# Optimization experiments

Hardware: AMD Instinct MI355X
Metric: run time of the kernel (lower is better)

Reference implementation:

```python
import jax, jax.numpy as jnp
import numpy as np

L, H, D, DH, DFF, V, P, T, R = 12, 12, 768, 64, 3072, 30522, 512, 2, 50
RAT_LAYER = 6  # original condition: 5 < idx < 7


def layer_norm(x, g, b, eps=1e-12):
    m = x.mean(-1, keepdims=True)
    v = ((x - m) ** 2).mean(-1, keepdims=True)
    return (x - m) / jnp.sqrt(v + eps) * g + b


def setup_inputs() -> dict:
    key = jax.random.key(0)
    ks = iter(jax.random.split(key, 20))
    def n(shape, s=0.02):
        return jax.random.normal(next(ks), shape, dtype=jnp.float32) * s
    inp = dict(
        input_ids=jax.random.randint(next(ks), (4, 512), 0, V, dtype=jnp.int32),
        relations=jax.random.randint(next(ks), (4, 512, 512), 0, R, dtype=jnp.int32),
        attention_mask=jnp.ones((4, 512), dtype=jnp.int32),
        word_emb=n((V, D)), pos_emb=n((P, D)), type_emb=n((T, D)),
        emb_ln_g=jnp.ones((D,)), emb_ln_b=jnp.zeros((D,)),
        Wq=n((L, D, D)), bq=jnp.zeros((L, D)), Wk=n((L, D, D)), bk=jnp.zeros((L, D)),
        Wv=n((L, D, D)), bv=jnp.zeros((L, D)), Wo=n((L, D, D)), bo=jnp.zeros((L, D)),
        ln1_g=jnp.ones((L, D)), ln1_b=jnp.zeros((L, D)),
        Wi=n((L, D, DFF)), bi=jnp.zeros((L, DFF)),
        Wf=n((L, DFF, D)), bf=jnp.zeros((L, D)),
        ln2_g=jnp.ones((L, D)), ln2_b=jnp.zeros((L, D)),
        key_rel=n((L, R, DH)), val_rel=n((L, R, DH)),
        pool_w=n((D, D)), pool_b=jnp.zeros((D,)),
    )
    return inp


def reference(input_ids, relations, attention_mask, word_emb, pos_emb, type_emb,
              emb_ln_g, emb_ln_b, Wq, bq, Wk, bk, Wv, bv, Wo, bo, ln1_g, ln1_b,
              Wi, bi, Wf, bf, ln2_g, ln2_b, key_rel, val_rel, pool_w, pool_b):
    B, S = input_ids.shape
    # BERT embeddings (token_type_ids = zeros as in module default)
    h = word_emb[input_ids] + pos_emb[jnp.arange(S)][None] + type_emb[0][None, None]
    h = layer_norm(h, emb_ln_g, emb_ln_b)
    ext_mask = (1.0 - attention_mask.astype(jnp.float32))[:, None, None, :] * -10000.0
    inv_sqrt_dh = np.float32(1.0 / np.sqrt(DH))
    for i in range(L):
        q = (h @ Wq[i] + bq[i]).reshape(B, S, H, DH).transpose(0, 2, 1, 3)
        k = (h @ Wk[i] + bk[i]).reshape(B, S, H, DH).transpose(0, 2, 1, 3)
        v = (h @ Wv[i] + bv[i]).reshape(B, S, H, DH).transpose(0, 2, 1, 3)
        scores = jnp.einsum('bhsd,bhtd->bhst', q, k)
        if i == RAT_LAYER:
            kr = key_rel[i][relations]            # [B,S,S,DH] gathered relation keys
            scores = scores + jnp.einsum('bhsd,bstd->bhst', q, kr)
        scores = scores * inv_sqrt_dh + ext_mask
        probs = jax.nn.softmax(scores, axis=-1)   # dropout = identity (eval)
        ctx = jnp.einsum('bhst,bhtd->bhsd', probs, v)
        if i == RAT_LAYER:
            vr = val_rel[i][relations]            # [B,S,S,DH] gathered relation values
            ctx = ctx + jnp.einsum('bhst,bstd->bhsd', probs, vr)
        ctx = ctx.transpose(0, 2, 1, 3).reshape(B, S, D)
        attn_out = layer_norm(ctx @ Wo[i] + bo[i] + h, ln1_g[i], ln1_b[i])
        ff = jax.nn.gelu(attn_out @ Wi[i] + bi[i], approximate=False)
        h = layer_norm(ff @ Wf[i] + bf[i] + attn_out, ln2_g[i], ln2_b[i])
    pooled = jnp.tanh(h[:, 0] @ pool_w + pool_b)
    return h, pooled
```

## Files before the change

kernel.cpp:

```cpp
#include <hip/hip_runtime.h>
#include <math.h>

typedef unsigned short u16;
typedef unsigned int   u32;
typedef __bf16  bf16x8 __attribute__((ext_vector_type(8)));
typedef float   f32x4  __attribute__((ext_vector_type(4)));
typedef u16     u16x8  __attribute__((ext_vector_type(8)));

__device__ __forceinline__ u16 f2bf(float f) {
  u32 u = __builtin_bit_cast(u32, f);
  u32 r = (u + 0x7fffu + ((u >> 16) & 1u)) >> 16;
  return (u16)r;
}
__device__ __forceinline__ float bf2f(u16 h) {
  u32 u = ((u32)h) << 16;
  return __builtin_bit_cast(float, u);
}
__device__ __forceinline__ void gload16(const void* g, void* l) {
  __builtin_amdgcn_global_load_lds((const __attribute__((address_space(1))) void*)g,
                                   (__attribute__((address_space(3))) void*)l, 16, 0, 0);
}
__device__ __forceinline__ bf16x8 ld_bf8(const u16* p) {
  u16x8 v = *(const u16x8*)p;
  return __builtin_bit_cast(bf16x8, v);
}
__device__ __forceinline__ f32x4 mfma16(bf16x8 a, bf16x8 b, f32x4 c) {
  return __builtin_amdgcn_mfma_f32_16x16x32_bf16(a, b, c, 0, 0, 0);
}

struct ConvP {
  const float *wq, *wk, *wv, *wo, *wi, *wf;
  u16 *oqkv, *oo, *oi, *of;
};
__global__ __launch_bounds__(256) void conv_weights(ConvP p) {
  int t = blockIdx.x;
  const float* in; u16* out; int K, N, tn, tk;
  if (t < 1728) { int wh = t / 576, tt = t % 576;
    in = wh==0 ? p.wq : (wh==1 ? p.wk : p.wv);
    out = p.oqkv + (size_t)wh * 768 * 768;
    K = 768; N = 768; tn = tt % 24; tk = tt / 24;
  } else if (t < 2304) { int tt = t - 1728; in = p.wo; out = p.oo; K=768;  N=768;  tn=tt%24; tk=tt/24; }
  else if (t < 4608)   { int tt = t - 2304; in = p.wi; out = p.oi; K=768;  N=3072; tn=tt%96; tk=tt/96; }
  else                 { int tt = t - 4608; in = p.wf; out = p.of; K=3072; N=768;  tn=tt%24; tk=tt/24; }
  int n0 = tn*32, k0 = tk*32;
  __shared__ float tile[32][33];
  int x = threadIdx.x, y = threadIdx.y;
  #pragma unroll
  for (int j = 0; j < 4; ++j)
    tile[y + j*8][x] = in[(size_t)(k0 + y + j*8) * N + n0 + x];
  __syncthreads();
  #pragma unroll
  for (int j = 0; j < 4; ++j)
    out[(size_t)(n0 + y + j*8) * K + k0 + x] = f2bf(tile[x][y + j*8]);
}

struct GP {
  const u16* A; const u16* B;
  int K, N;
  long sA, sB, sOut;
  const float* bias; const float* res;
  float* outF; u16* outB;
  const float* bq; const float* bk; const float* bv;
  u16* qO; u16* kO; u16* vO;
};

template<int BM, int BN, int WAVES, int EPI, int KS>
__global__ __launch_bounds__(WAVES*64) void gemm_bt(GP p) {
  constexpr int THREADS = WAVES * 64;
  constexpr int WC = WAVES / 2;
  constexpr int WM = BM / 2, WN = BN / WC, MR = WM / 16, NR = WN / 16;
  constexpr int AIT = BM * 64 / (THREADS * 8);
  constexpr int BIT = BN * 64 / (THREADS * 8);
  const int tid = threadIdx.x;
  const int wave = tid >> 6, lane = tid & 63;
  const int wr = wave / WC, wc = wave % WC;
  const int wm0 = wr * WM, wn0 = wc * WN;
  const int bn = blockIdx.x, bm = blockIdx.y, bz = blockIdx.z;
  const int K = p.K;
  const int kLen = K / KS;
  const int kBeg = (KS > 1) ? bz * kLen : 0;
  const u16* A  = p.A + ((KS > 1) ? 0 : (size_t)bz * p.sA);
  const u16* Bp = p.B + ((KS > 1) ? 0 : (size_t)bz * p.sB);
  const int rowA0 = bm * BM, colB0 = bn * BN;

  __shared__ __align__(16) u16 lds[(BM + BN) * 64];
  u16* Al = lds; u16* Bl = lds + BM * 64;

  f32x4 acc[MR][NR];
  #pragma unroll
  for (int i = 0; i < MR; ++i)
    #pragma unroll
    for (int j = 0; j < NR; ++j) acc[i][j] = f32x4{0.f,0.f,0.f,0.f};

  for (int kt = kBeg; kt < kBeg + kLen; kt += 64) {
    #pragma unroll
    for (int it = 0; it < AIT; ++it) {
      int e = tid * 8 + it * THREADS * 8;
      gload16(A + (size_t)(rowA0 + (e >> 6)) * K + kt + (e & 63), Al + e);
    }
    #pragma unroll
    for (int it = 0; it < BIT; ++it) {
      int e = tid * 8 + it * THREADS * 8;
      gload16(Bp + (size_t)(colB0 + (e >> 6)) * K + kt + (e & 63), Bl + e);
    }
    __syncthreads();
    #pragma unroll
    for (int ks = 0; ks < 2; ++ks) {
      bf16x8 av[MR]; bf16x8 bw[NR];
      #pragma unroll
      for (int mf = 0; mf < MR; ++mf)
        av[mf] = ld_bf8(Al + (wm0 + mf*16 + (lane&15))*64 + ks*32 + (lane>>4)*8);
      #pragma unroll
      for (int nf = 0; nf < NR; ++nf)
        bw[nf] = ld_bf8(Bl + (wn0 + nf*16 + (lane&15))*64 + ks*32 + (lane>>4)*8);
      #pragma unroll
      for (int mf = 0; mf < MR; ++mf)
        #pragma unroll
        for (int nf = 0; nf < NR; ++nf)
          acc[mf][nf] = mfma16(av[mf], bw[nf], acc[mf][nf]);
    }
    __syncthreads();
  }

  #pragma unroll
  for (int mf = 0; mf < MR; ++mf) {
    #pragma unroll
    for (int nf = 0; nf < NR; ++nf) {
      int col = colB0 + wn0 + nf*16 + (lane & 15);
      #pragma unroll
      for (int reg = 0; reg < 4; ++reg) {
        int row = rowA0 + wm0 + mf*16 + (lane >> 4)*4 + reg;
        float v = acc[mf][nf][reg];
        if constexpr (EPI == 0) {
          int wh = col / 768, cc = col % 768;
          int hh = cc >> 6, d = col & 63;
          int b = row >> 9, s = row & 511;
          const float* bias = wh==0 ? p.bq : (wh==1 ? p.bk : p.bv);
          u16 o = f2bf(v + bias[cc]);
          if (wh == 0)      p.qO[((((size_t)b*12 + hh)*512 + s) << 6) + d] = o;
          else if (wh == 1) p.kO[((((size_t)b*12 + hh)*512 + s) << 6) + d] = o;
          else              p.vO[((((size_t)b*12 + hh)*64  + d) << 9) + s] = o;
        } else if constexpr (EPI == 2) {
          p.outF[(size_t)bz * p.sOut + (size_t)row * p.N + col] = v;
        } else {
          float xg = v + p.bias[col];
          float gg = 0.5f * xg * (1.f + erff(xg * 0.70710678118f));
          p.outB[(size_t)row * p.N + col] = f2bf(gg);
        }
      }
    }
  }
}

template<int RAT>
__global__ __launch_bounds__(256) void flash_attn(
    const u16* __restrict__ q, const u16* __restrict__ k, const u16* __restrict__ v,
    const int* __restrict__ mask, u16* __restrict__ ctx,
    const float* __restrict__ qr, const int* __restrict__ rel,
    float* __restrict__ wbins) {
  const int head = blockIdx.x;
  const int bm = blockIdx.y;
  const int b = head / 12, hh = head % 12;
  const int tid = threadIdx.x, wave = tid >> 6, lane = tid & 63;
  const int row0 = bm * 64;
  const u16* qb = q + (size_t)head * 512 * 64;
  const u16* kb = k + (size_t)head * 512 * 64;
  const u16* vb = v + (size_t)head * 64 * 512;

  __shared__ __align__(16) u16 Ql[64*64];
  __shared__ __align__(16) u16 Kl[2][64*64];
  __shared__ __align__(16) u16 Vl[2][64*64];
  __shared__ __align__(16) u16 pw[4][16*72];
  __shared__ float em_lds[512];
  __shared__ float ll[64];
  __shared__ float qlds[RAT ? 64 : 1][RAT ? 52 : 1];
  __shared__ float wlds[RAT ? 64 : 1][RAT ? 52 : 1];
  __shared__ float scl[RAT ? 64 : 1];

  for (int i = tid; i < 512; i += 256)
    em_lds[i] = -10000.f * (1.f - (float)mask[b*512 + i]);
  #pragma unroll
  for (int it = 0; it < 2; ++it) {
    int e = tid*8 + it*2048;
    gload16(qb + (size_t)(row0 + (e>>6))*64 + (e&63), Ql + e);
  }
  #pragma unroll
  for (int it = 0; it < 2; ++it) {
    int e = tid*8 + it*2048;
    gload16(kb + (size_t)(e>>6)*64 + (e&63), Kl[0] + e);
    gload16(vb + (size_t)(e>>6)*512 + (e&63), Vl[0] + e);
  }
  if constexpr (RAT) {
    for (int i = tid; i < 64*52; i += 256) ((float*)wlds)[i] = 0.f;
    for (int i = tid; i < 64*50; i += 256) {
      int rr = i % 50, sr = i / 50;
      qlds[sr][rr] = qr[((size_t)head*512 + row0 + sr)*50 + rr];
    }
  }
  __syncthreads();

  bf16x8 qf[2];
  #pragma unroll
  for (int ks = 0; ks < 2; ++ks)
    qf[ks] = ld_bf8(Ql + (wave*16 + (lane&15))*64 + ks*32 + (lane>>4)*8);

  f32x4 ctxacc[4];
  #pragma unroll
  for (int nf = 0; nf < 4; ++nf) ctxacc[nf] = f32x4{0.f,0.f,0.f,0.f};
  float mrun[4], lrun[4];
  #pragma unroll
  for (int r = 0; r < 4; ++r) { mrun[r] = -3.0e38f; lrun[r] = 0.f; }

  for (int t0 = 0; t0 < 8; ++t0) {
    const int cur = t0 & 1;
    if (t0 < 7) {
      int t1 = (t0 + 1) * 64;
      #pragma unroll
      for (int it = 0; it < 2; ++it) {
        int e = tid*8 + it*2048;
        gload16(kb + (size_t)(t1 + (e>>6))*64 + (e&63), Kl[1-cur] + e);
        gload16(vb + (size_t)(e>>6)*512 + t1 + (e&63), Vl[1-cur] + e);
      }
    }

    f32x4 s[4];
    #pragma unroll
    for (int nf = 0; nf < 4; ++nf) s[nf] = f32x4{0.f,0.f,0.f,0.f};
    #pragma unroll
    for (int ks = 0; ks < 2; ++ks)
      #pragma unroll
      for (int nf = 0; nf < 4; ++nf) {
        bf16x8 kf = ld_bf8(Kl[cur] + (nf*16 + (lane&15))*64 + ks*32 + (lane>>4)*8);
        s[nf] = mfma16(qf[ks], kf, s[nf]);
      }

    u32 rr4[RAT ? 4 : 1];
    if constexpr (RAT) {
      #pragma unroll
      for (int nf = 0; nf < 4; ++nf) {
        int tt = t0*64 + nf*16 + (lane&15);
        u32 pack = 0;
        #pragma unroll
        for (int reg = 0; reg < 4; ++reg) {
          int rl = wave*16 + (lane>>4)*4 + reg;
          int rr = rel[((size_t)(b*512 + row0 + rl))*512 + tt];
          pack |= (u32)rr << (8*reg);
          s[nf][reg] += qlds[rl][rr];
        }
        rr4[nf] = pack;
      }
    }

    float em4[4];
    #pragma unroll
    for (int nf = 0; nf < 4; ++nf) em4[nf] = em_lds[t0*64 + nf*16 + (lane&15)];

    float scale_[4];
    #pragma unroll
    for (int reg = 0; reg < 4; ++reg) {
      float pm = -3.0e38f;
      #pragma unroll
      for (int nf = 0; nf < 4; ++nf) {
        s[nf][reg] = s[nf][reg]*0.125f + em4[nf];
        pm = fmaxf(pm, s[nf][reg]);
      }
      #pragma unroll
      for (int o = 1; o < 16; o <<= 1) pm = fmaxf(pm, __shfl_xor(pm, o));
      float mnew = fmaxf(mrun[reg], pm);
      float sc = __expf(mrun[reg] - mnew);
      mrun[reg] = mnew;
      scale_[reg] = sc;
      float lsum = 0.f;
      #pragma unroll
      for (int nf = 0; nf < 4; ++nf) {
        float e = __expf(s[nf][reg] - mnew);
        s[nf][reg] = e;
        lsum += e;
      }
      #pragma unroll
      for (int o = 1; o < 16; o <<= 1) lsum += __shfl_xor(lsum, o);
      lrun[reg] = lrun[reg]*sc + lsum;
      if constexpr (RAT) {
        if ((lane & 15) == 0) scl[wave*16 + (lane>>4)*4 + reg] = sc;
      }
    }

    if constexpr (RAT) {
      for (int i = lane; i < 16*50; i += 64) {
        int r = i / 50, bn = i % 50;
        wlds[wave*16 + r][bn] *= scl[wave*16 + r];
      }
      #pragma unroll
      for (int nf = 0; nf < 4; ++nf)
        #pragma unroll
        for (int reg = 0; reg < 4; ++reg) {
          int rl = wave*16 + (lane>>4)*4 + reg;
          int rr = (rr4[nf] >> (8*reg)) & 255;
          atomicAdd(&wlds[rl][rr], s[nf][reg]);
        }
    }

    #pragma unroll
    for (int nf = 0; nf < 4; ++nf)
      #pragma unroll
      for (int reg = 0; reg < 4; ++reg) {
        int qq = (lane>>4)*4 + reg;
        pw[wave][qq*72 + nf*16 + (lane&15)] = f2bf(s[nf][reg]);
      }

    #pragma unroll
    for (int nf = 0; nf < 4; ++nf)
      #pragma unroll
      for (int reg = 0; reg < 4; ++reg)
        ctxacc[nf][reg] *= scale_[reg];
    #pragma unroll
    for (int ks = 0; ks < 2; ++ks) {
      bf16x8 pf = ld_bf8(pw[wave] + (lane&15)*72 + ks*32 + (lane>>4)*8);
      #pragma unroll
      for (int nf = 0; nf < 4; ++nf) {
        bf16x8 vf = ld_bf8(Vl[cur] + (nf*16 + (lane&15))*64 + ks*32 + (lane>>4)*8);
        ctxacc[nf] = mfma16(pf, vf, ctxacc[nf]);
      }
    }
    __syncthreads();
  }

  #pragma unroll
  for (int nf = 0; nf < 4; ++nf)
    #pragma unroll
    for (int reg = 0; reg < 4; ++reg) {
      int qg = row0 + wave*16 + (lane>>4)*4 + reg;
      int d  = nf*16 + (lane&15);
      ctx[((size_t)(b*512 + qg))*768 + hh*64 + d] = f2bf(ctxacc[nf][reg] / lrun[reg]);
    }

  if constexpr (RAT) {
    if ((lane & 15) == 0) {
      #pragma unroll
      for (int reg = 0; reg < 4; ++reg)
        ll[wave*16 + (lane>>4)*4 + reg] = lrun[reg];
    }
    __syncthreads();
    for (int i = tid; i < 64*50; i += 256) {
      int rr = i % 50, sr = i / 50;
      wbins[((size_t)head*512 + row0 + sr)*50 + rr] = wlds[sr][rr] / ll[sr];
    }
  }
}

__global__ __launch_bounds__(256) void rat_qr(const u16* __restrict__ q,
    const float* __restrict__ kr, float* __restrict__ qr) {
  int idx = blockIdx.x * 256 + threadIdx.x;
  if (idx >= 24576 * 50) return;
  int r = idx % 50; size_t bhs = (size_t)idx / 50;
  const u16* qp = q + bhs * 64;
  const float* kp = kr + r * 64;
  float acc = 0.f;
  #pragma unroll
  for (int d = 0; d < 64; ++d) acc += bf2f(qp[d]) * kp[d];
  qr[idx] = acc;
}

__global__ __launch_bounds__(256) void rat_apply(const float* __restrict__ wbins,
    const float* __restrict__ vr, u16* __restrict__ ctx) {
  __shared__ float vrl[50*64];
  __shared__ float wl[32*50];
  int tid = threadIdx.x;
  int rows0 = blockIdx.x * 32;
  for (int i = tid; i < 50*64; i += 256) vrl[i] = vr[i];
  for (int i = tid; i < 32*50; i += 256) wl[i] = wbins[(size_t)rows0*50 + i];
  __syncthreads();
  int wave = tid >> 6, lane = tid & 63;
  #pragma unroll
  for (int i = 0; i < 8; ++i) {
    int r = wave*8 + i;
    size_t idx = (size_t)rows0 + r;
    float acc = 0.f;
    #pragma unroll
    for (int j = 0; j < 50; ++j) acc += wl[r*50 + j] * vrl[j*64 + lane];
    int s = (int)(idx & 511); size_t bh = idx >> 9;
    int b = (int)(bh / 12), hh = (int)(bh % 12);
    u16* cp = ctx + ((size_t)(b*512 + s))*768 + hh*64 + lane;
    *cp = f2bf(bf2f(*cp) + acc);
  }
}

__global__ __launch_bounds__(256) void embed_ln(const int* __restrict__ ids,
    const float* __restrict__ we, const float* __restrict__ pe, const float* __restrict__ te,
    const float* __restrict__ g, const float* __restrict__ b,
    float* __restrict__ hF, u16* __restrict__ hB) {
  int row = blockIdx.x, tid = threadIdx.x;
  int s = row & 511;
  int id = ids[row];
  float x[3];
  #pragma unroll
  for (int j = 0; j < 3; ++j) {
    int d = tid + j*256;
    x[j] = we[(size_t)id*768 + d] + pe[(size_t)s*768 + d] + te[d];
  }
  __shared__ float red[4];
  float sm = x[0] + x[1] + x[2];
  #pragma unroll
  for (int o = 32; o; o >>= 1) sm += __shfl_xor(sm, o);
  if (!(tid & 63)) red[tid >> 6] = sm;
  __syncthreads();
  float mean = (red[0]+red[1]+red[2]+red[3]) * (1.f/768.f);
  __syncthreads();
  float q = 0.f;
  #pragma unroll
  for (int j = 0; j < 3; ++j) { float d = x[j] - mean; q += d*d; }
  #pragma unroll
  for (int o = 32; o; o >>= 1) q += __shfl_xor(q, o);
  if (!(tid & 63)) red[tid >> 6] = q;
  __syncthreads();
  float inv = rsqrtf((red[0]+red[1]+red[2]+red[3]) * (1.f/768.f) + 1e-12f);
  #pragma unroll
  for (int j = 0; j < 3; ++j) {
    int d = tid + j*256;
    float y = (x[j] - mean) * inv * g[d] + b[d];
    hF[(size_t)row*768 + d] = y;
    hB[(size_t)row*768 + d] = f2bf(y);
  }
}

__global__ __launch_bounds__(256) void ln_fused(const float* __restrict__ p0,
    const float* __restrict__ p1, const float* __restrict__ p2, const float* __restrict__ p3,
    int np, const float* __restrict__ bias, const float* __restrict__ res,
    const float* __restrict__ g, const float* __restrict__ b,
    float* __restrict__ oF, u16* __restrict__ oB) {
  int row = blockIdx.x, tid = threadIdx.x;
  size_t base = (size_t)row * 768;
  float v[3];
  #pragma unroll
  for (int j = 0; j < 3; ++j) {
    int d = tid + j*256;
    float x = p0[base + d];
    if (np > 1) x += p1[base + d];
    if (np > 2) x += p2[base + d];
    if (np > 3) x += p3[base + d];
    v[j] = x + bias[d] + res[base + d];
  }
  __shared__ float red[4];
  float sm = v[0] + v[1] + v[2];
  #pragma unroll
  for (int o = 32; o; o >>= 1) sm += __shfl_xor(sm, o);
  if (!(tid & 63)) red[tid >> 6] = sm;
  __syncthreads();
  float mean = (red[0]+red[1]+red[2]+red[3]) * (1.f/768.f);
  __syncthreads();
  float q = 0.f;
  #pragma unroll
  for (int j = 0; j < 3; ++j) { float d = v[j] - mean; q += d*d; }
  #pragma unroll
  for (int o = 32; o; o >>= 1) q += __shfl_xor(q, o);
  if (!(tid & 63)) red[tid >> 6] = q;
  __syncthreads();
  float inv = rsqrtf((red[0]+red[1]+red[2]+red[3]) * (1.f/768.f) + 1e-12f);
  #pragma unroll
  for (int j = 0; j < 3; ++j) {
    int d = tid + j*256;
    float y = (v[j] - mean) * inv * g[d] + b[d];
    oF[base + d] = y;
    oB[base + d] = f2bf(y);
  }
}

__global__ __launch_bounds__(256) void pooler_k(const float* __restrict__ h,
    const float* __restrict__ w, const float* __restrict__ bias, float* __restrict__ out) {
  int b = blockIdx.x, tid = threadIdx.x;
  __shared__ float hr[768];
  for (int i = tid; i < 768; i += 256) hr[i] = h[((size_t)b*512)*768 + i];
  __syncthreads();
  float a0 = 0.f, a1 = 0.f, a2 = 0.f;
  for (int kk = 0; kk < 768; ++kk) {
    float hv = hr[kk];
    const float* wr = w + (size_t)kk*768;
    a0 += hv * wr[tid]; a1 += hv * wr[tid+256]; a2 += hv * wr[tid+512];
  }
  out[(size_t)b*768 + tid]       = tanhf(a0 + bias[tid]);
  out[(size_t)b*768 + tid + 256] = tanhf(a1 + bias[tid+256]);
  out[(size_t)b*768 + tid + 512] = tanhf(a2 + bias[tid+512]);
}

__global__ __launch_bounds__(256) void copy_out(const float* __restrict__ in, float* __restrict__ out) {
  size_t i = ((size_t)blockIdx.x * 256 + threadIdx.x) * 4;
  *(float4*)(out + i) = *(const float4*)(in + i);
}

extern "C" void kernel_launch(void* const* d_in, const int* in_sizes, int n_in,
                              void* d_out, int out_size, void* d_ws, size_t ws_size,
                              hipStream_t stream) {
  const int*   ids   = (const int*)d_in[0];
  const int*   rel   = (const int*)d_in[1];
  const int*   amask = (const int*)d_in[2];
  const float* we    = (const float*)d_in[3];
  const float* pe    = (const float*)d_in[4];
  const float* te    = (const float*)d_in[5];
  const float* eg    = (const float*)d_in[6];
  const float* ebb   = (const float*)d_in[7];
  const float* Wq    = (const float*)d_in[8];
  const float* bq    = (const float*)d_in[9];
  const float* Wk    = (const float*)d_in[10];
  const float* bk    = (const float*)d_in[11];
  const float* Wv    = (const float*)d_in[12];
  const float* bv    = (const float*)d_in[13];
  const float* Wo    = (const float*)d_in[14];
  const float* bo    = (const float*)d_in[15];
  const float* g1    = (const float*)d_in[16];
  const float* b1    = (const float*)d_in[17];
  const float* Wi    = (const float*)d_in[18];
  const float* bi    = (const float*)d_in[19];
  const float* Wf    = (const float*)d_in[20];
  const float* bfp   = (const float*)d_in[21];
  const float* g2    = (const float*)d_in[22];
  const float* b2    = (const float*)d_in[23];
  const float* krel  = (const float*)d_in[24];
  const float* vrel  = (const float*)d_in[25];
  const float* pwp   = (const float*)d_in[26];
  const float* pbp   = (const float*)d_in[27];
  (void)in_sizes; (void)n_in; (void)out_size; (void)ws_size;

  char* ws = (char*)d_ws;
  size_t off = 0;
  auto take = [&](size_t bytes) { char* p = ws + off; off += (bytes + 255) & ~(size_t)255; return p; };
  u16*   wqkv = (u16*)take((size_t)2304*768*2);
  u16*   wo_l = (u16*)take((size_t)768*768*2);
  u16*   wi_l = (u16*)take((size_t)3072*768*2);
  u16*   wf_l = (u16*)take((size_t)768*3072*2);
  float* hF   = (float*)take((size_t)2048*768*4);
  u16*   hB   = (u16*)take((size_t)2048*768*2);
  float* atF  = (float*)take((size_t)2048*768*4);
  u16*   atB  = (u16*)take((size_t)2048*768*2);
  u16*   qB   = (u16*)take((size_t)2048*768*2);
  u16*   kB   = (u16*)take((size_t)2048*768*2);
  u16*   vB   = (u16*)take((size_t)2048*768*2);
  u16*   ctxB = (u16*)take((size_t)2048*768*2);
  float* tmpF = (float*)take((size_t)4*2048*768*4);
  u16*   ffB  = (u16*)take((size_t)2048*3072*2);
  float* qrF  = (float*)take((size_t)24576*50*4);
  float* wbF  = (float*)take((size_t)24576*50*4);
  const size_t PSTRIDE = (size_t)2048*768;

  embed_ln<<<2048, 256, 0, stream>>>(ids, we, pe, te, eg, ebb, hF, hB);

  for (int l = 0; l < 12; ++l) {
    ConvP cp{Wq + (size_t)l*768*768, Wk + (size_t)l*768*768, Wv + (size_t)l*768*768,
             Wo + (size_t)l*768*768, Wi + (size_t)l*768*3072, Wf + (size_t)l*3072*768,
             wqkv, wo_l, wi_l, wf_l};
    conv_weights<<<6912, dim3(32,8), 0, stream>>>(cp);

    GP pq{}; pq.A = hB; pq.B = wqkv; pq.K = 768; pq.N = 2304;
    pq.bq = bq + l*768; pq.bk = bk + l*768; pq.bv = bv + l*768;
    pq.qO = qB; pq.kO = kB; pq.vO = vB;
    gemm_bt<128,128,8,0,1><<<dim3(18,16,1), 512, 0, stream>>>(pq);

    if (l == 6) {
      rat_qr<<<4800, 256, 0, stream>>>(qB, krel + 6*50*64, qrF);
      flash_attn<1><<<dim3(48,8), 256, 0, stream>>>(qB, kB, vB, amask, ctxB, qrF, rel, wbF);
      rat_apply<<<768, 256, 0, stream>>>(wbF, vrel + 6*50*64, ctxB);
    } else {
      flash_attn<0><<<dim3(48,8), 256, 0, stream>>>(qB, kB, vB, amask, ctxB, nullptr, nullptr, nullptr);
    }

    GP po{}; po.A = ctxB; po.B = wo_l; po.K = 768; po.N = 768; po.sOut = PSTRIDE;
    po.outF = tmpF;
    gemm_bt<64,128,4,2,2><<<dim3(6,32,2), 256, 0, stream>>>(po);
    ln_fused<<<2048, 256, 0, stream>>>(tmpF, tmpF + PSTRIDE, nullptr, nullptr, 2,
                                       bo + l*768, hF, g1 + l*768, b1 + l*768, atF, atB);

    GP pf1{}; pf1.A = atB; pf1.B = wi_l; pf1.K = 768; pf1.N = 3072;
    pf1.bias = bi + (size_t)l*3072; pf1.outB = ffB;
    gemm_bt<128,128,8,3,1><<<dim3(24,16,1), 512, 0, stream>>>(pf1);

    GP pf2{}; pf2.A = ffB; pf2.B = wf_l; pf2.K = 3072; pf2.N = 768; pf2.sOut = PSTRIDE;
    pf2.outF = tmpF;
    gemm_bt<64,128,4,2,4><<<dim3(6,32,4), 256, 0, stream>>>(pf2);
    ln_fused<<<2048, 256, 0, stream>>>(tmpF, tmpF + PSTRIDE, tmpF + 2*PSTRIDE, tmpF + 3*PSTRIDE, 4,
                                       bfp + l*768, atF, g2 + l*768, b2 + l*768, hF, hB);
  }

  copy_out<<<1536, 256, 0, stream>>>(hF, (float*)d_out);
  pooler_k<<<4, 256, 0, stream>>>(hF, pwp, pbp, (float*)d_out + (size_t)2048*768);
}
```

Measured before the change: 1.943 ms.

## Split flash attention KV range across two wave groups and merge softmax states

Flash attention blocks grow from 256 to 512 threads: each 16-row query group gets two waves that each handle half of the 512 keys, and their partial max/sum/context (and relation bins) are merged at the end through shared memory. Q is loaded straight into registers, and K/V tiles use an XOR-swizzled LDS layout to cut bank conflicts. The double-buffered prefetch is replaced by a load, sync, compute loop, which removes load/compute overlap. It also adds a merge phase and more shared-memory use in exchange for more waves in flight per block.

```diff
diff --git a/kernel.cpp b/kernel.cpp
--- a/kernel.cpp
+++ b/kernel.cpp
@@ -153,7 +153,7 @@
 }
 
 template<int RAT>
-__global__ __launch_bounds__(256) void flash_attn(
+__global__ __launch_bounds__(512) void flash_attn(
     const u16* __restrict__ q, const u16* __restrict__ k, const u16* __restrict__ v,
     const int* __restrict__ mask, u16* __restrict__ ctx,
     const float* __restrict__ qr, const int* __restrict__ rel,
@@ -162,47 +162,36 @@
   const int bm = blockIdx.y;
   const int b = head / 12, hh = head % 12;
   const int tid = threadIdx.x, wave = tid >> 6, lane = tid & 63;
+  const int wr = wave >> 1, wc = wave & 1;
   const int row0 = bm * 64;
   const u16* qb = q + (size_t)head * 512 * 64;
   const u16* kb = k + (size_t)head * 512 * 64;
   const u16* vb = v + (size_t)head * 64 * 512;
 
-  __shared__ __align__(16) u16 Ql[64*64];
   __shared__ __align__(16) u16 Kl[2][64*64];
   __shared__ __align__(16) u16 Vl[2][64*64];
-  __shared__ __align__(16) u16 pw[4][16*72];
+  __shared__ __align__(16) u16 pw[8][16*72];
   __shared__ float em_lds[512];
-  __shared__ float ll[64];
+  __shared__ float mlb[4][16][2];
   __shared__ float qlds[RAT ? 64 : 1][RAT ? 52 : 1];
-  __shared__ float wlds[RAT ? 64 : 1][RAT ? 52 : 1];
-  __shared__ float scl[RAT ? 64 : 1];
-
-  for (int i = tid; i < 512; i += 256)
-    em_lds[i] = -10000.f * (1.f - (float)mask[b*512 + i]);
-  #pragma unroll
-  for (int it = 0; it < 2; ++it) {
-    int e = tid*8 + it*2048;
-    gload16(qb + (size_t)(row0 + (e>>6))*64 + (e&63), Ql + e);
-  }
-  #pragma unroll
-  for (int it = 0; it < 2; ++it) {
-    int e = tid*8 + it*2048;
-    gload16(kb + (size_t)(e>>6)*64 + (e&63), Kl[0] + e);
-    gload16(vb + (size_t)(e>>6)*512 + (e&63), Vl[0] + e);
-  }
+  __shared__ float wlds[RAT ? 2 : 1][RAT ? 64 : 1][RAT ? 50 : 1];
+  __shared__ float scl[RAT ? 2 : 1][RAT ? 64 : 1];
+  __shared__ float aex[RAT ? 64 : 1][RAT ? 3 : 1];
+
+  em_lds[tid] = -10000.f * (1.f - (float)mask[b*512 + tid]);
   if constexpr (RAT) {
-    for (int i = tid; i < 64*52; i += 256) ((float*)wlds)[i] = 0.f;
-    for (int i = tid; i < 64*50; i += 256) {
+    for (int i = tid; i < 2*64*50; i += 512) ((float*)wlds)[i] = 0.f;
+    for (int i = tid; i < 64*50; i += 512) {
       int rr = i % 50, sr = i / 50;
       qlds[sr][rr] = qr[((size_t)head*512 + row0 + sr)*50 + rr];
     }
   }
-  __syncthreads();
-
+
+  const int qrow = row0 + wr*16 + (lane & 15);
   bf16x8 qf[2];
-  #pragma unroll
-  for (int ks = 0; ks < 2; ++ks)
-    qf[ks] = ld_bf8(Ql + (wave*16 + (lane&15))*64 + ks*32 + (lane>>4)*8);
+  qf[0] = ld_bf8(qb + (size_t)qrow*64 +      (lane>>4)*8);
+  qf[1] = ld_bf8(qb + (size_t)qrow*64 + 32 + (lane>>4)*8);
+  __syncthreads();
 
   f32x4 ctxacc[4];
   #pragma unroll
@@ -211,17 +200,18 @@
   #pragma unroll
   for (int r = 0; r < 4; ++r) { mrun[r] = -3.0e38f; lrun[r] = 0.f; }
 
-  for (int t0 = 0; t0 < 8; ++t0) {
-    const int cur = t0 & 1;
-    if (t0 < 7) {
-      int t1 = (t0 + 1) * 64;
-      #pragma unroll
-      for (int it = 0; it < 2; ++it) {
-        int e = tid*8 + it*2048;
-        gload16(kb + (size_t)(t1 + (e>>6))*64 + (e&63), Kl[1-cur] + e);
-        gload16(vb + (size_t)(e>>6)*512 + t1 + (e&63), Vl[1-cur] + e);
-      }
-    }
+  const int g = lane >> 4;
+  for (int it = 0; it < 4; ++it) {
+    {
+      int prow = tid >> 3, lcol = (tid & 7) ^ (prow & 7);
+      int t0a = it*64, t0b = 256 + it*64;
+      gload16(kb + (size_t)(t0a + prow)*64 + lcol*8, Kl[0] + tid*8);
+      gload16(kb + (size_t)(t0b + prow)*64 + lcol*8, Kl[1] + tid*8);
+      gload16(vb + (size_t)prow*512 + t0a + lcol*8, Vl[0] + tid*8);
+      gload16(vb + (size_t)prow*512 + t0b + lcol*8, Vl[1] + tid*8);
+    }
+    __syncthreads();
+    const int tbase = wc*256 + it*64;
 
     f32x4 s[4];
     #pragma unroll
@@ -230,7 +220,9 @@
     for (int ks = 0; ks < 2; ++ks)
       #pragma unroll
       for (int nf = 0; nf < 4; ++nf) {
-        bf16x8 kf = ld_bf8(Kl[cur] + (nf*16 + (lane&15))*64 + ks*32 + (lane>>4)*8);
+        int row = nf*16 + (lane & 15);
+        int c16 = (ks*4 + g) ^ (row & 7);
+        bf16x8 kf = ld_bf8(Kl[wc] + row*64 + c16*8);
         s[nf] = mfma16(qf[ks], kf, s[nf]);
       }
 
@@ -238,11 +230,11 @@
     if constexpr (RAT) {
       #pragma unroll
       for (int nf = 0; nf < 4; ++nf) {
-        int tt = t0*64 + nf*16 + (lane&15);
+        int tt = tbase + nf*16 + (lane & 15);
         u32 pack = 0;
         #pragma unroll
         for (int reg = 0; reg < 4; ++reg) {
-          int rl = wave*16 + (lane>>4)*4 + reg;
+          int rl = wr*16 + (lane>>4)*4 + reg;
           int rr = rel[((size_t)(b*512 + row0 + rl))*512 + tt];
           pack |= (u32)rr << (8*reg);
           s[nf][reg] += qlds[rl][rr];
@@ -253,7 +245,7 @@
 
     float em4[4];
     #pragma unroll
-    for (int nf = 0; nf < 4; ++nf) em4[nf] = em_lds[t0*64 + nf*16 + (lane&15)];
+    for (int nf = 0; nf < 4; ++nf) em4[nf] = em_lds[tbase + nf*16 + (lane & 15)];
 
     float scale_[4];
     #pragma unroll
@@ -281,22 +273,22 @@
       for (int o = 1; o < 16; o <<= 1) lsum += __shfl_xor(lsum, o);
       lrun[reg] = lrun[reg]*sc + lsum;
       if constexpr (RAT) {
-        if ((lane & 15) == 0) scl[wave*16 + (lane>>4)*4 + reg] = sc;
+        if ((lane & 15) == 0) scl[wc][wr*16 + (lane>>4)*4 + reg] = sc;
       }
     }
 
     if constexpr (RAT) {
       for (int i = lane; i < 16*50; i += 64) {
-        int r = i / 50, bn = i % 50;
-        wlds[wave*16 + r][bn] *= scl[wave*16 + r];
+        int r = i / 50;
+        wlds[wc][wr*16 + r][i % 50] *= scl[wc][wr*16 + r];
       }
       #pragma unroll
       for (int nf = 0; nf < 4; ++nf)
         #pragma unroll
         for (int reg = 0; reg < 4; ++reg) {
-          int rl = wave*16 + (lane>>4)*4 + reg;
+          int rl = wr*16 + (lane>>4)*4 + reg;
           int rr = (rr4[nf] >> (8*reg)) & 255;
-          atomicAdd(&wlds[rl][rr], s[nf][reg]);
+          atomicAdd(&wlds[wc][rl][rr], s[nf][reg]);
         }
     }
 
@@ -305,7 +297,7 @@
       #pragma unroll
       for (int reg = 0; reg < 4; ++reg) {
         int qq = (lane>>4)*4 + reg;
-        pw[wave][qq*72 + nf*16 + (lane&15)] = f2bf(s[nf][reg]);
+        pw[wave][qq*72 + nf*16 + (lane & 15)] = f2bf(s[nf][reg]);
       }
 
     #pragma unroll
@@ -315,35 +307,70 @@
         ctxacc[nf][reg] *= scale_[reg];
     #pragma unroll
     for (int ks = 0; ks < 2; ++ks) {
-      bf16x8 pf = ld_bf8(pw[wave] + (lane&15)*72 + ks*32 + (lane>>4)*8);
+      bf16x8 pf = ld_bf8(pw[wave] + (lane & 15)*72 + ks*32 + g*8);
       #pragma unroll
       for (int nf = 0; nf < 4; ++nf) {
-        bf16x8 vf = ld_bf8(Vl[cur] + (nf*16 + (lane&15))*64 + ks*32 + (lane>>4)*8);
+        int row = nf*16 + (lane & 15);
+        int c16 = (ks*4 + g) ^ (row & 7);
+        bf16x8 vf = ld_bf8(Vl[wc] + row*64 + c16*8);
         ctxacc[nf] = mfma16(pf, vf, ctxacc[nf]);
       }
     }
     __syncthreads();
   }
 
-  #pragma unroll
-  for (int nf = 0; nf < 4; ++nf)
+  float* mergeF = (float*)pw;
+  if (wc == 1) {
+    #pragma unroll
+    for (int nf = 0; nf < 4; ++nf)
+      #pragma unroll
+      for (int reg = 0; reg < 4; ++reg)
+        mergeF[(wr*16 + (lane>>4)*4 + reg)*66 + nf*16 + (lane & 15)] = ctxacc[nf][reg];
+    if ((lane & 15) == 0) {
+      #pragma unroll
+      for (int reg = 0; reg < 4; ++reg) {
+        mlb[wr][(lane>>4)*4 + reg][0] = mrun[reg];
+        mlb[wr][(lane>>4)*4 + reg][1] = lrun[reg];
+      }
+    }
+  }
+  __syncthreads();
+  if (wc == 0) {
+    float a1[4], a2[4], linv[4];
     #pragma unroll
     for (int reg = 0; reg < 4; ++reg) {
-      int qg = row0 + wave*16 + (lane>>4)*4 + reg;
-      int d  = nf*16 + (lane&15);
-      ctx[((size_t)(b*512 + qg))*768 + hh*64 + d] = f2bf(ctxacc[nf][reg] / lrun[reg]);
-    }
-
+      int r = (lane>>4)*4 + reg;
+      float m2 = mlb[wr][r][0], l2 = mlb[wr][r][1];
+      float mn = fmaxf(mrun[reg], m2);
+      a1[reg] = __expf(mrun[reg] - mn);
+      a2[reg] = __expf(m2 - mn);
+      linv[reg] = 1.f / (lrun[reg]*a1[reg] + l2*a2[reg]);
+      if constexpr (RAT) {
+        if ((lane & 15) == 0) {
+          aex[wr*16 + r][0] = a1[reg];
+          aex[wr*16 + r][1] = a2[reg];
+          aex[wr*16 + r][2] = linv[reg];
+        }
+      }
+    }
+    #pragma unroll
+    for (int nf = 0; nf < 4; ++nf)
+      #pragma unroll
+      for (int reg = 0; reg < 4; ++reg) {
+        int r = wr*16 + (lane>>4)*4 + reg;
+        int qg = row0 + r;
+        int d = nf*16 + (lane & 15);
+        float v2 = mergeF[r*66 + d];
+        ctx[((size_t)(b*512 + qg))*768 + hh*64 + d] =
+            f2bf((ctxacc[nf][reg]*a1[reg] + v2*a2[reg]) * linv[reg]);
+      }
+  }
   if constexpr (RAT) {
-    if ((lane & 15) == 0) {
-      #pragma unroll
-      for (int reg = 0; reg < 4; ++reg)
-        ll[wave*16 + (lane>>4)*4 + reg] = lrun[reg];
-    }
     __syncthreads();
-    for (int i = tid; i < 64*50; i += 256) {
-      int rr = i % 50, sr = i / 50;
-      wbins[((size_t)head*512 + row0 + sr)*50 + rr] = wlds[sr][rr] / ll[sr];
+    for (int i = tid; i < 64*50; i += 512) {
+      int sr = i / 50, rr = i % 50;
+      wbins[((size_t)head*512 + row0 + sr)*50 + rr] =
+          (wlds[0][sr][rr]*aex[sr][0] + wlds[1][sr][rr]*aex[sr][1]) * aex[sr][2];
     }
   }
 }
@@ -556,10 +583,10 @@
 
     if (l == 6) {
       rat_qr<<<4800, 256, 0, stream>>>(qB, krel + 6*50*64, qrF);
-      flash_attn<1><<<dim3(48,8), 256, 0, stream>>>(qB, kB, vB, amask, ctxB, qrF, rel, wbF);
+      flash_attn<1><<<dim3(48,8), 512, 0, stream>>>(qB, kB, vB, amask, ctxB, qrF, rel, wbF);
       rat_apply<<<768, 256, 0, stream>>>(wbF, vrel + 6*50*64, ctxB);
     } else {
-      flash_attn<0><<<dim3(48,8), 256, 0, stream>>>(qB, kB, vB, amask, ctxB, nullptr, nullptr, nullptr);
+      flash_attn<0><<<dim3(48,8), 512, 0, stream>>>(qB, kB, vB, amask, ctxB, nullptr, nullptr, nullptr);
     }
 
     GP po{}; po.A = ctxB; po.B = wo_l; po.K = 768; po.N = 768; po.sOut = PSTRIDE;
```

After: 1.888 ms. 1.03x faster.
